# Kernel tuning notes

Measured on AMD Instinct MI355X. Metric: run time of the kernel, lower is better.

The kernel has to match this reference:

```python
import jax, jax.numpy as jnp
import numpy as np

D = 128  # node_dim (hardcoded in the torch module)


def _bn(x, g, b, eps=1e-5):
    # BatchNorm1d in training mode: per-batch mean / biased variance
    m = x.mean(0)
    v = x.var(0)
    return (x - m) * jax.lax.rsqrt(v + eps) * g + b


def setup_inputs() -> dict:
    key = jax.random.key(0)
    ks = jax.random.split(key, 16)
    N, E, ED = 4096, 16384, 16
    node = jax.random.normal(ks[0], (N, D), jnp.float32)
    edge = jax.random.normal(ks[1], (E, ED), jnp.float32)
    hidden = jax.random.normal(ks[2], (1, N, D), jnp.float32)
    edge_index = jax.random.randint(ks[3], (E, 2), 0, N)

    def lin(k, o, i):
        return jax.random.normal(k, (o, i), jnp.float32) / np.sqrt(i).astype(np.float32)

    W1 = lin(ks[4], 256, ED)
    W2 = lin(ks[5], 256, 256)
    W3 = lin(ks[6], 128, 256)
    W4 = lin(ks[7], D * D, 128)
    g1, b1 = jnp.ones(256), jnp.zeros(256)
    g2, b2 = jnp.ones(256), jnp.zeros(256)
    g3, b3 = jnp.ones(128), jnp.zeros(128)
    g4, b4 = jnp.ones(D * D), jnp.zeros(D * D)
    lim = 1.0 / np.sqrt(D).astype(np.float32)
    bias = jax.random.uniform(ks[8], (D,), jnp.float32, -lim, lim)
    W_ih = lin(ks[9], 3 * D, D)
    W_hh = lin(ks[10], 3 * D, D)
    b_ih = jnp.zeros(3 * D)
    b_hh = jnp.zeros(3 * D)
    return dict(node=node, edge_index=edge_index, edge=edge, hidden=hidden,
                W1=W1, g1=g1, b1=b1, W2=W2, g2=g2, b2=b2, W3=W3, g3=g3, b3=b3,
                W4=W4, g4=g4, b4=b4, bias=bias, W_ih=W_ih, W_hh=W_hh,
                b_ih=b_ih, b_hh=b_hh)


def reference(node, edge_index, edge, hidden, W1, g1, b1, W2, g2, b2,
              W3, g3, b3, W4, g4, b4, bias, W_ih, W_hh, b_ih, b_hh):
    N = node.shape[0]
    E = edge.shape[0]
    h0 = hidden[0]  # [N, D]
    src, dst = edge_index[:, 0], edge_index[:, 1]

    # edge encoder -> per-edge [D, D] weight matrix
    x = jax.nn.relu(_bn(edge @ W1.T, g1, b1))
    x = jax.nn.relu(_bn(x @ W2.T, g2, b2))
    x = jax.nn.relu(_bn(x @ W3.T, g3, b3))
    w = _bn(x @ W4.T, g4, b4).reshape(E, D, D)

    # gather source nodes, per-edge vector-matrix product
    x_i = node[src]                               # [E, D]
    msg = jnp.einsum('ed,edk->ek', x_i, w)        # [E, D]

    # scatter-mean over destination nodes
    sums = jax.ops.segment_sum(msg, dst, num_segments=N)
    cnt = jax.ops.segment_sum(jnp.ones((E, 1), msg.dtype), dst, num_segments=N)
    message = sums / jnp.maximum(cnt, 1.0)
    m = jax.nn.relu(message + bias)               # [N, D]

    # single-step GRU (PyTorch gate order r, z, n)
    gi = m @ W_ih.T + b_ih
    gh = h0 @ W_hh.T + b_hh
    r = jax.nn.sigmoid(gi[:, :D] + gh[:, :D])
    z = jax.nn.sigmoid(gi[:, D:2 * D] + gh[:, D:2 * D])
    n = jnp.tanh(gi[:, 2 * D:] + r * gh[:, 2 * D:])
    hn = (1.0 - z) * n + z * h0                   # [N, D]
    return hn, hn[None]
```

## Files before the change

kernel.cpp:

```cpp
#include <hip/hip_runtime.h>

#define EPS 1e-5f

typedef _Float16 half8 __attribute__((ext_vector_type(8)));
typedef float f32x16 __attribute__((ext_vector_type(16)));

__global__ __launch_bounds__(256) void gemm_abt(const float* __restrict__ A,
                                                const float* __restrict__ B,
                                                float* __restrict__ C,
                                                int M, int N, int K,
                                                float* __restrict__ osum,
                                                float* __restrict__ osq) {
  __shared__ float As[16][68];
  __shared__ float Bs[16][68];
  const int t = threadIdx.x;
  const int tx = t & 15, ty = t >> 4;
  const int m0 = blockIdx.y * 64, n0 = blockIdx.x * 64;
  float acc[4][4] = {};
  for (int k0 = 0; k0 < K; k0 += 16) {
    __syncthreads();
    {
      const int r = t >> 2;
      const int kk = (t & 3) << 2;
      float4 av = *(const float4*)&A[(size_t)(m0 + r) * K + k0 + kk];
      As[kk + 0][r] = av.x; As[kk + 1][r] = av.y;
      As[kk + 2][r] = av.z; As[kk + 3][r] = av.w;
      float4 bv = *(const float4*)&B[(size_t)(n0 + r) * K + k0 + kk];
      Bs[kk + 0][r] = bv.x; Bs[kk + 1][r] = bv.y;
      Bs[kk + 2][r] = bv.z; Bs[kk + 3][r] = bv.w;
    }
    __syncthreads();
#pragma unroll
    for (int kk = 0; kk < 16; ++kk) {
      float4 a = *(const float4*)&As[kk][ty << 2];
      float4 b = *(const float4*)&Bs[kk][tx << 2];
      float av[4] = {a.x, a.y, a.z, a.w};
      float bv[4] = {b.x, b.y, b.z, b.w};
#pragma unroll
      for (int i = 0; i < 4; ++i)
#pragma unroll
        for (int j = 0; j < 4; ++j) acc[i][j] += av[i] * bv[j];
    }
  }
#pragma unroll
  for (int i = 0; i < 4; ++i) {
    float4 o = make_float4(acc[i][0], acc[i][1], acc[i][2], acc[i][3]);
    *(float4*)&C[(size_t)(m0 + (ty << 2) + i) * N + n0 + (tx << 2)] = o;
  }
  __syncthreads();
  float* sred = (float*)As;
  if (t < 128) sred[t] = 0.f;
  __syncthreads();
#pragma unroll
  for (int j = 0; j < 4; ++j) {
    float s = 0.f, sq = 0.f;
#pragma unroll
    for (int i = 0; i < 4; ++i) {
      float v = acc[i][j];
      s += v; sq += v * v;
    }
    atomicAdd(&sred[((tx << 2) + j) * 2 + 0], s);
    atomicAdd(&sred[((tx << 2) + j) * 2 + 1], sq);
  }
  __syncthreads();
  if (t < 64) {
    atomicAdd(&osum[n0 + t], sred[t * 2]);
    atomicAdd(&osq[n0 + t], sred[t * 2 + 1]);
  }
}

template <int TRANS, bool STATS>
__global__ __launch_bounds__(256) void gemm16(const float* __restrict__ A,
                                              const float* __restrict__ B,
                                              float* __restrict__ C,
                                              int lda, int ldb, int ldc, int K,
                                              const float* __restrict__ s1,
                                              const float* __restrict__ s2,
                                              const float* __restrict__ g,
                                              const float* __restrict__ b,
                                              float invM,
                                              float* __restrict__ osum,
                                              float* __restrict__ osq) {
  __shared__ _Float16 As[128 * 64];
  __shared__ _Float16 Bs[128 * 64];
  __shared__ float scL[256], shL[256];
  const int t = threadIdx.x;
  const int m0 = blockIdx.y * 128, n0 = blockIdx.x * 128;
  const int w = t >> 6, l = t & 63;
  const int wm = w >> 1, wn = w & 1;
  const int lr = l & 31, lg = l >> 5;
  if (TRANS == 1) {
    if (t < K) {
      float mean = s1[t] * invM;
      float var = s2[t] * invM - mean * mean;
      float sc = g[t] * rsqrtf(var + EPS);
      scL[t] = sc;
      shL[t] = b[t] - mean * sc;
    }
  }
  f32x16 acc[2][2];
#pragma unroll
  for (int i = 0; i < 2; ++i)
#pragma unroll
    for (int j = 0; j < 2; ++j) acc[i][j] = (f32x16){0.f};
  for (int k0 = 0; k0 < K; k0 += 64) {
    __syncthreads();
#pragma unroll
    for (int i = 0; i < 4; ++i) {
      const int gq = i * 256 + t;
      const int f = gq >> 6, lp = gq & 63;
      const int row = (f >> 2) * 32 + (lp & 31);
      const int c = (f & 3) * 16 + (lp >> 5) * 8;
      const float* ap = A + (size_t)(m0 + row) * lda + k0 + c;
      float4 a4 = *(const float4*)ap, b4 = *(const float4*)(ap + 4);
      float va[8] = {a4.x, a4.y, a4.z, a4.w, b4.x, b4.y, b4.z, b4.w};
      if (TRANS == 1) {
#pragma unroll
        for (int j = 0; j < 8; ++j)
          va[j] = fmaxf(va[j] * scL[k0 + c + j] + shL[k0 + c + j], 0.f);
      }
      half8 h;
#pragma unroll
      for (int j = 0; j < 8; ++j) h[j] = (_Float16)va[j];
      *(half8*)(As + (size_t)gq * 8) = h;
      const float* bp = B + (size_t)(n0 + row) * ldb + k0 + c;
      float4 e4 = *(const float4*)bp, f4 = *(const float4*)(bp + 4);
      half8 hb;
      hb[0] = (_Float16)e4.x; hb[1] = (_Float16)e4.y; hb[2] = (_Float16)e4.z; hb[3] = (_Float16)e4.w;
      hb[4] = (_Float16)f4.x; hb[5] = (_Float16)f4.y; hb[6] = (_Float16)f4.z; hb[7] = (_Float16)f4.w;
      *(half8*)(Bs + (size_t)gq * 8) = hb;
    }
    __syncthreads();
#pragma unroll
    for (int ks = 0; ks < 4; ++ks) {
      half8 af[2], bf[2];
#pragma unroll
      for (int mb = 0; mb < 2; ++mb) {
        af[mb] = *(const half8*)(As + (size_t)(((wm * 2 + mb) * 4 + ks) * 64 + l) * 8);
        bf[mb] = *(const half8*)(Bs + (size_t)(((wn * 2 + mb) * 4 + ks) * 64 + l) * 8);
      }
#pragma unroll
      for (int mb = 0; mb < 2; ++mb)
#pragma unroll
        for (int nb = 0; nb < 2; ++nb)
          acc[mb][nb] = __builtin_amdgcn_mfma_f32_32x32x16_f16(af[mb], bf[nb], acc[mb][nb], 0, 0, 0);
    }
  }
#pragma unroll
  for (int mb = 0; mb < 2; ++mb)
#pragma unroll
    for (int nb = 0; nb < 2; ++nb)
#pragma unroll
      for (int r = 0; r < 16; ++r) {
        const int row = m0 + wm * 64 + mb * 32 + (r & 3) + 8 * (r >> 2) + 4 * lg;
        const int col = n0 + wn * 64 + nb * 32 + lr;
        C[(size_t)row * ldc + col] = acc[mb][nb][r];
      }
  if (STATS) {
    __syncthreads();
    float* sred = (float*)As;
    if (t < 256) sred[t] = 0.f;
    __syncthreads();
#pragma unroll
    for (int nb = 0; nb < 2; ++nb) {
      float s = 0.f, sq = 0.f;
#pragma unroll
      for (int mb = 0; mb < 2; ++mb)
#pragma unroll
        for (int r = 0; r < 16; ++r) {
          float v = acc[mb][nb][r];
          s += v; sq += v * v;
        }
      const int cl = wn * 64 + nb * 32 + lr;
      atomicAdd(&sred[cl * 2 + 0], s);
      atomicAdd(&sred[cl * 2 + 1], sq);
    }
    __syncthreads();
    if (t < 128) {
      atomicAdd(&osum[n0 + t], sred[t * 2]);
      atomicAdd(&osq[n0 + t], sred[t * 2 + 1]);
    }
  }
}

__global__ __launch_bounds__(256) void gram_kernel(const float* __restrict__ y3,
                                                   float* __restrict__ part,
                                                   const float* __restrict__ s3sum,
                                                   const float* __restrict__ s3sq,
                                                   const float* __restrict__ g3,
                                                   const float* __restrict__ b3,
                                                   float invE,
                                                   float* __restrict__ colsum) {
  __shared__ float xL[128 * 132];
  __shared__ float scL[128], shL[128];
  const int t = threadIdx.x, tx = t & 15, ty = t >> 4;
  if (t < 128) {
    float mean = s3sum[t] * invE;
    float var = s3sq[t] * invE - mean * mean;
    float sc = g3[t] * rsqrtf(var + EPS);
    scL[t] = sc;
    shL[t] = b3[t] - mean * sc;
  }
  __syncthreads();
  const int r0 = blockIdx.x * 128;
#pragma unroll
  for (int i = 0; i < 16; ++i) {
    int f4 = t + i * 256;
    int r = f4 >> 5;
    int c4 = (f4 & 31) << 2;
    float4 v = *(const float4*)&y3[(size_t)(r0 + r) * 128 + c4];
    v.x = fmaxf(v.x * scL[c4 + 0] + shL[c4 + 0], 0.f);
    v.y = fmaxf(v.y * scL[c4 + 1] + shL[c4 + 1], 0.f);
    v.z = fmaxf(v.z * scL[c4 + 2] + shL[c4 + 2], 0.f);
    v.w = fmaxf(v.w * scL[c4 + 3] + shL[c4 + 3], 0.f);
    *(float4*)&xL[r * 132 + c4] = v;
  }
  __syncthreads();
  float acc[8][8] = {};
  float csum[8] = {};
  for (int r = 0; r < 128; ++r) {
    float4 a0 = *(const float4*)&xL[r * 132 + ty * 8];
    float4 a1 = *(const float4*)&xL[r * 132 + ty * 8 + 4];
    float4 b0 = *(const float4*)&xL[r * 132 + tx * 8];
    float4 b1 = *(const float4*)&xL[r * 132 + tx * 8 + 4];
    float a[8] = {a0.x, a0.y, a0.z, a0.w, a1.x, a1.y, a1.z, a1.w};
    float b[8] = {b0.x, b0.y, b0.z, b0.w, b1.x, b1.y, b1.z, b1.w};
#pragma unroll
    for (int i = 0; i < 8; ++i)
#pragma unroll
      for (int j = 0; j < 8; ++j) acc[i][j] += a[i] * b[j];
    if (tx == ty) {
#pragma unroll
      for (int i = 0; i < 8; ++i) csum[i] += a[i];
    }
  }
  float* base = part + (size_t)blockIdx.x * 16384;
#pragma unroll
  for (int i = 0; i < 8; ++i)
#pragma unroll
    for (int j = 0; j < 8; ++j)
      base[(ty * 8 + i) * 128 + tx * 8 + j] = acc[i][j];
  if (tx == ty) {
#pragma unroll
    for (int i = 0; i < 8; ++i) atomicAdd(&colsum[ty * 8 + i], csum[i]);
  }
}

__global__ __launch_bounds__(256) void gram_reduce(const float* __restrict__ part,
                                                   float* __restrict__ out) {
  int idx = blockIdx.x * 256 + threadIdx.x;
  float s = 0.f;
  for (int b = 0; b < 128; ++b) s += part[(size_t)b * 16384 + idx];
  out[idx] = s;
}

__global__ __launch_bounds__(256) void w4_finalize(const float* __restrict__ W4,
                                                   const float* __restrict__ U,
                                                   const float* __restrict__ colsum3,
                                                   const float* __restrict__ g4,
                                                   const float* __restrict__ b4,
                                                   _Float16* __restrict__ BTf,
                                                   float* __restrict__ t4,
                                                   float invM) {
  const int r = (blockIdx.x * 256 + threadIdx.x) >> 6;
  const int lane = threadIdx.x & 63;
  const float* wp = W4 + (size_t)r * 128;
  const float* up = U + (size_t)r * 128;
  float p1 = 0.f, p2 = 0.f;
#pragma unroll
  for (int c0 = 0; c0 < 128; c0 += 64) {
    float wv = wp[c0 + lane];
    p1 += up[c0 + lane] * wv;
    p2 += colsum3[c0 + lane] * wv;
  }
#pragma unroll
  for (int off = 32; off > 0; off >>= 1) {
    p1 += __shfl_down(p1, off);
    p2 += __shfl_down(p2, off);
  }
  p1 = __shfl(p1, 0);
  p2 = __shfl(p2, 0);
  float m4 = p2 * invM;
  float q = p1 * invM;
  float s = g4[r] * rsqrtf(q - m4 * m4 + EPS);
  if (lane == 0) t4[r] = b4[r] - m4 * s;
  const int kout = r & 127, d = r >> 7;
  if (lane < 16) {
    const int ks = lane >> 1, lg = lane & 1;
    const float* cp = wp + lane * 8;
    float4 va = *(const float4*)cp, vb = *(const float4*)(cp + 4);
    half8 h;
    h[0] = (_Float16)(s * va.x); h[1] = (_Float16)(s * va.y);
    h[2] = (_Float16)(s * va.z); h[3] = (_Float16)(s * va.w);
    h[4] = (_Float16)(s * vb.x); h[5] = (_Float16)(s * vb.y);
    h[6] = (_Float16)(s * vb.z); h[7] = (_Float16)(s * vb.w);
    size_t off16 = (size_t)d * 16384 +
                   (size_t)((((kout >> 5) * 8 + ks) * 64) + (kout & 31) + lg * 32) * 8;
    *(half8*)(BTf + off16) = h;
  }
}

__global__ __launch_bounds__(256, 2) void zgemm(const float* __restrict__ y3,
                                                const float* __restrict__ node,
                                                const int* __restrict__ eidx,
                                                const _Float16* __restrict__ BTf,
                                                const float* __restrict__ Tn,
                                                const float* __restrict__ s3sum,
                                                const float* __restrict__ s3sq,
                                                const float* __restrict__ g3,
                                                const float* __restrict__ b3,
                                                float invE,
                                                float* __restrict__ sums) {
  __shared__ __align__(16) _Float16 Bs[2][16384];
  __shared__ _Float16 xiL[32 * 128];
  __shared__ float scL[128], shL[128];
  const int t = threadIdx.x;
  const int e0 = blockIdx.y * 128;
  const int d0 = blockIdx.x * 32;
  const int w = t >> 6, l = t & 63;
  const int wm = w >> 1, wn = w & 1;
  const int lr = l & 31, lg = l >> 5;
  if (t < 128) {
    float mean = s3sum[t] * invE;
    float var = s3sq[t] * invE - mean * mean;
    float sc = g3[t] * rsqrtf(var + EPS);
    scL[t] = sc;
    shL[t] = b3[t] - mean * sc;
  }
  {
    const int e = t >> 1, db = (t & 1) * 16;
    const int src = eidx[(e0 + e) * 2];
    const float* np = node + (size_t)src * 128 + d0 + db;
#pragma unroll
    for (int j = 0; j < 16; j += 4) {
      float4 v = *(const float4*)(np + j);
      xiL[(db + j + 0) * 128 + e] = (_Float16)v.x;
      xiL[(db + j + 1) * 128 + e] = (_Float16)v.y;
      xiL[(db + j + 2) * 128 + e] = (_Float16)v.z;
      xiL[(db + j + 3) * 128 + e] = (_Float16)v.w;
    }
  }
  half8 st[8];
  {
    const _Float16* p = BTf + (size_t)d0 * 16384 + (size_t)t * 8;
#pragma unroll
    for (int j = 0; j < 8; ++j) st[j] = *(const half8*)(p + j * 2048);
  }
  __syncthreads();
  half8 xf[2][8];
#pragma unroll
  for (int mb = 0; mb < 2; ++mb) {
    const float* xp = y3 + (size_t)(e0 + wm * 64 + mb * 32 + lr) * 128 + lg * 8;
#pragma unroll
    for (int ks = 0; ks < 8; ++ks) {
      const int c = ks * 16 + lg * 8;
      float4 a = *(const float4*)(xp + ks * 16);
      float4 b = *(const float4*)(xp + ks * 16 + 4);
      float va[8] = {a.x, a.y, a.z, a.w, b.x, b.y, b.z, b.w};
      half8 h;
#pragma unroll
      for (int j = 0; j < 8; ++j)
        h[j] = (_Float16)fmaxf(va[j] * scL[c + j] + shL[c + j], 0.f);
      xf[mb][ks] = h;
    }
  }
  f32x16 acc00 = (f32x16){0.f}, acc01 = (f32x16){0.f};
  f32x16 acc10 = (f32x16){0.f}, acc11 = (f32x16){0.f};

  for (int dt = 0; dt < 32; ++dt) {
    _Float16* bs = &Bs[dt & 1][0];
#pragma unroll
    for (int j = 0; j < 8; ++j) *(half8*)(bs + t * 8 + j * 2048) = st[j];
    if (dt < 31) {
      const _Float16* p = BTf + (size_t)(d0 + dt + 1) * 16384 + (size_t)t * 8;
#pragma unroll
      for (int j = 0; j < 8; ++j) st[j] = *(const half8*)(p + j * 2048);
    }
    asm volatile("s_waitcnt lgkmcnt(0)" ::: "memory");
    __builtin_amdgcn_s_barrier();
    const _Float16 xv0 = xiL[dt * 128 + wm * 64 + lr];
    const _Float16 xv1 = xiL[dt * 128 + wm * 64 + 32 + lr];
    const half8 xb0 = {xv0, xv0, xv0, xv0, xv0, xv0, xv0, xv0};
    const half8 xb1 = {xv1, xv1, xv1, xv1, xv1, xv1, xv1, xv1};
    __builtin_amdgcn_s_setprio(1);
#pragma unroll
    for (int ks = 0; ks < 8; ++ks) {
      half8 b0 = *(const half8*)(bs + (size_t)(((wn * 2 + 0) * 8 + ks) * 64 + l) * 8);
      half8 b1 = *(const half8*)(bs + (size_t)(((wn * 2 + 1) * 8 + ks) * 64 + l) * 8);
      half8 a0 = xf[0][ks] * xb0;
      half8 a1 = xf[1][ks] * xb1;
      acc00 = __builtin_amdgcn_mfma_f32_32x32x16_f16(a0, b0, acc00, 0, 0, 0);
      acc01 = __builtin_amdgcn_mfma_f32_32x32x16_f16(a0, b1, acc01, 0, 0, 0);
      acc10 = __builtin_amdgcn_mfma_f32_32x32x16_f16(a1, b0, acc10, 0, 0, 0);
      acc11 = __builtin_amdgcn_mfma_f32_32x32x16_f16(a1, b1, acc11, 0, 0, 0);
    }
    __builtin_amdgcn_s_setprio(0);
  }
  const bool add_t = (blockIdx.x == 0);
#pragma unroll
  for (int r = 0; r < 16; ++r) {
    const int rl = (r & 3) + 8 * (r >> 2) + 4 * lg;
    const int eA = e0 + wm * 64 + rl;
    const int eB = eA + 32;
    const int dA = eidx[eA * 2 + 1], sA = eidx[eA * 2];
    const int dB = eidx[eB * 2 + 1], sB = eidx[eB * 2];
    const int c0 = wn * 64 + lr;
    float v00 = acc00[r], v01 = acc01[r], v10 = acc10[r], v11 = acc11[r];
    if (add_t) {
      v00 += Tn[(size_t)sA * 128 + c0];
      v01 += Tn[(size_t)sA * 128 + c0 + 32];
      v10 += Tn[(size_t)sB * 128 + c0];
      v11 += Tn[(size_t)sB * 128 + c0 + 32];
    }
    atomicAdd(&sums[(size_t)dA * 128 + c0], v00);
    atomicAdd(&sums[(size_t)dA * 128 + c0 + 32], v01);
    atomicAdd(&sums[(size_t)dB * 128 + c0], v10);
    atomicAdd(&sums[(size_t)dB * 128 + c0 + 32], v11);
  }
}

__global__ __launch_bounds__(128) void t4n_kernel(const float* __restrict__ node,
                                                  const float* __restrict__ t4,
                                                  float* __restrict__ Tn,
                                                  const int* __restrict__ eidx,
                                                  float* __restrict__ cnt, int E) {
  __shared__ float nodeL[8][128];
  const int k = threadIdx.x;
  const int n0 = blockIdx.x * 8;
  {
    int e = blockIdx.x * 32 + k;
    if (k < 32 && e < E) atomicAdd(&cnt[eidx[e * 2 + 1]], 1.0f);
  }
#pragma unroll
  for (int j = 0; j < 8; ++j) nodeL[j][k] = node[(size_t)(n0 + j) * 128 + k];
  __syncthreads();
  float acc[8] = {};
  for (int d = 0; d < 128; ++d) {
    float wv = t4[d * 128 + k];
#pragma unroll
    for (int j = 0; j < 8; ++j) acc[j] += nodeL[j][d] * wv;
  }
#pragma unroll
  for (int j = 0; j < 8; ++j) Tn[(size_t)(n0 + j) * 128 + k] = acc[j];
}

__global__ __launch_bounds__(256) void gru_gates(const float* __restrict__ sums,
                                                 const float* __restrict__ cnt,
                                                 const float* __restrict__ bias,
                                                 const float* __restrict__ h0,
                                                 const float* __restrict__ Wih,
                                                 const float* __restrict__ Whh,
                                                 float* __restrict__ gi,
                                                 float* __restrict__ gh) {
  __shared__ _Float16 As[128 * 64];
  __shared__ _Float16 Bs[128 * 64];
  const bool isgh = blockIdx.x >= 3;
  const float* A = isgh ? h0 : sums;
  const float* B = isgh ? Whh : Wih;
  float* C = isgh ? gh : gi;
  const int n0 = (isgh ? blockIdx.x - 3 : blockIdx.x) * 128;
  const int m0 = blockIdx.y * 128;
  const int t = threadIdx.x;
  const int w = t >> 6, l = t & 63;
  const int wm = w >> 1, wn = w & 1;
  const int lr = l & 31, lg = l >> 5;
  f32x16 acc[2][2];
#pragma unroll
  for (int i = 0; i < 2; ++i)
#pragma unroll
    for (int j = 0; j < 2; ++j) acc[i][j] = (f32x16){0.f};
  for (int k0 = 0; k0 < 128; k0 += 64) {
    __syncthreads();
#pragma unroll
    for (int i = 0; i < 4; ++i) {
      const int gq = i * 256 + t;
      const int f = gq >> 6, lp = gq & 63;
      const int row = (f >> 2) * 32 + (lp & 31);
      const int c = (f & 3) * 16 + (lp >> 5) * 8;
      const float* ap = A + (size_t)(m0 + row) * 128 + k0 + c;
      float4 a4 = *(const float4*)ap, b4 = *(const float4*)(ap + 4);
      float va[8] = {a4.x, a4.y, a4.z, a4.w, b4.x, b4.y, b4.z, b4.w};
      if (!isgh) {
        float rc = 1.f / fmaxf(cnt[m0 + row], 1.f);
#pragma unroll
        for (int j = 0; j < 8; ++j) va[j] = fmaxf(va[j] * rc + bias[k0 + c + j], 0.f);
      }
      half8 h;
#pragma unroll
      for (int j = 0; j < 8; ++j) h[j] = (_Float16)va[j];
      *(half8*)(As + (size_t)gq * 8) = h;
      const float* bp = B + (size_t)(n0 + row) * 128 + k0 + c;
      float4 e4 = *(const float4*)bp, f4 = *(const float4*)(bp + 4);
      half8 hb;
      hb[0] = (_Float16)e4.x; hb[1] = (_Float16)e4.y; hb[2] = (_Float16)e4.z; hb[3] = (_Float16)e4.w;
      hb[4] = (_Float16)f4.x; hb[5] = (_Float16)f4.y; hb[6] = (_Float16)f4.z; hb[7] = (_Float16)f4.w;
      *(half8*)(Bs + (size_t)gq * 8) = hb;
    }
    __syncthreads();
#pragma unroll
    for (int ks = 0; ks < 4; ++ks) {
      half8 af[2], bf[2];
#pragma unroll
      for (int mb = 0; mb < 2; ++mb) {
        af[mb] = *(const half8*)(As + (size_t)(((wm * 2 + mb) * 4 + ks) * 64 + l) * 8);
        bf[mb] = *(const half8*)(Bs + (size_t)(((wn * 2 + mb) * 4 + ks) * 64 + l) * 8);
      }
#pragma unroll
      for (int mb = 0; mb < 2; ++mb)
#pragma unroll
        for (int nb = 0; nb < 2; ++nb)
          acc[mb][nb] = __builtin_amdgcn_mfma_f32_32x32x16_f16(af[mb], bf[nb], acc[mb][nb], 0, 0, 0);
    }
  }
#pragma unroll
  for (int mb = 0; mb < 2; ++mb)
#pragma unroll
    for (int nb = 0; nb < 2; ++nb)
#pragma unroll
      for (int r = 0; r < 16; ++r) {
        const int row = m0 + wm * 64 + mb * 32 + (r & 3) + 8 * (r >> 2) + 4 * lg;
        const int col = n0 + wn * 64 + nb * 32 + lr;
        C[(size_t)row * 384 + col] = acc[mb][nb][r];
      }
}

__global__ __launch_bounds__(256) void gru_finalize(const float* __restrict__ gi,
                                                    const float* __restrict__ gh,
                                                    const float* __restrict__ h0,
                                                    const float* __restrict__ bih,
                                                    const float* __restrict__ bhh,
                                                    float* __restrict__ out, int Nn) {
  int idx = blockIdx.x * 256 + threadIdx.x;
  int n = idx >> 7, k = idx & 127;
  const float* gin = gi + (size_t)n * 384;
  const float* ghn = gh + (size_t)n * 384;
  float r = 1.f / (1.f + expf(-(gin[k] + bih[k] + ghn[k] + bhh[k])));
  float z = 1.f / (1.f + expf(-(gin[128 + k] + bih[128 + k] + ghn[128 + k] + bhh[128 + k])));
  float nn = tanhf(gin[256 + k] + bih[256 + k] + r * (ghn[256 + k] + bhh[256 + k]));
  float h = h0[idx];
  float hn = (1.f - z) * nn + z * h;
  out[idx] = hn;
  out[idx + (size_t)Nn * 128] = hn;
}

extern "C" void kernel_launch(void* const* d_in, const int* in_sizes, int n_in,
                              void* d_out, int out_size, void* d_ws, size_t ws_size,
                              hipStream_t stream) {
  const float* node = (const float*)d_in[0];
  const int* eidx = (const int*)d_in[1];
  const float* edge = (const float*)d_in[2];
  const float* hidden = (const float*)d_in[3];
  const float* W1 = (const float*)d_in[4];
  const float* g1 = (const float*)d_in[5];
  const float* b1 = (const float*)d_in[6];
  const float* W2 = (const float*)d_in[7];
  const float* g2 = (const float*)d_in[8];
  const float* b2 = (const float*)d_in[9];
  const float* W3 = (const float*)d_in[10];
  const float* g3 = (const float*)d_in[11];
  const float* b3 = (const float*)d_in[12];
  const float* W4 = (const float*)d_in[13];
  const float* g4 = (const float*)d_in[14];
  const float* b4 = (const float*)d_in[15];
  const float* bias = (const float*)d_in[16];
  const float* Wih = (const float*)d_in[17];
  const float* Whh = (const float*)d_in[18];
  const float* bih = (const float*)d_in[19];
  const float* bhh = (const float*)d_in[20];
  float* out = (float*)d_out;

  const int Nn = in_sizes[0] / 128;
  const int E = in_sizes[2] / 16;
  const float invE = 1.0f / (float)E;

  float* ws = (float*)d_ws;
  float* ybuf1 = ws + 0;
  float* ybuf2 = ws + 4194304;
  float* y3buf = ws + 8388608;
  _Float16* BTf = (_Float16*)(ws + 10485760);
  float* t4 = ws + 11534336;
  float* stats = ws + 11550720;
  float* G3 = ws + 11552512;
  float* sums = ws + 11568896;
  float* cnt = ws + 12093184;
  float* Tn = ws + 12097280;
  float* stat1 = stats, *stat2 = stats + 512, *stat3 = stats + 1024;
  float* colsum3 = stats + 1536;
  float* gpart = ybuf1;
  float* U = ybuf2;
  float* gi = ybuf2;
  float* gh = ybuf2 + 1572864;

  hipMemsetAsync(stats, 0, 1664 * sizeof(float), stream);
  hipMemsetAsync(sums, 0, ((size_t)Nn * 128 + Nn) * sizeof(float), stream);

  gemm_abt<<<dim3(4, E / 64), 256, 0, stream>>>(edge, W1, ybuf1, E, 256, 16, stat1, stat1 + 256);
  gemm16<1, true><<<dim3(2, E / 128), 256, 0, stream>>>(ybuf1, W2, ybuf2, 256, 256, 256, 256,
                                                        stat1, stat1 + 256, g1, b1, invE,
                                                        stat2, stat2 + 256);
  gemm16<1, true><<<dim3(1, E / 128), 256, 0, stream>>>(ybuf2, W3, y3buf, 256, 256, 128, 256,
                                                        stat2, stat2 + 256, g2, b2, invE,
                                                        stat3, stat3 + 256);

  gram_kernel<<<E / 128, 256, 0, stream>>>(y3buf, gpart, stat3, stat3 + 256, g3, b3, invE,
                                           colsum3);
  gram_reduce<<<64, 256, 0, stream>>>(gpart, G3);

  gemm16<0, false><<<dim3(1, 16384 / 128), 256, 0, stream>>>(W4, G3, U, 128, 128, 128, 128,
                                                             nullptr, nullptr, nullptr, nullptr,
                                                             0.f, nullptr, nullptr);
  w4_finalize<<<16384 / 4, 256, 0, stream>>>(W4, U, colsum3, g4, b4, BTf, t4, invE);
  t4n_kernel<<<Nn / 8, 128, 0, stream>>>(node, t4, Tn, eidx, cnt, E);

  zgemm<<<dim3(4, E / 128), 256, 0, stream>>>(y3buf, node, eidx, BTf, Tn,
                                              stat3, stat3 + 256, g3, b3, invE, sums);

  gru_gates<<<dim3(6, Nn / 128), 256, 0, stream>>>(sums, cnt, bias, hidden, Wih, Whh, gi, gh);
  gru_finalize<<<Nn * 128 / 256, 256, 0, stream>>>(gi, gh, hidden, bih, bhh, out, Nn);
}
```

Before: 254.9 us.

## Store edge-encoder intermediates in fp16 and restructure zgemm B-tile prefetch

The edge-encoder activations y1, y2 and y3 are now written as fp16 instead of fp32, and the downstream GEMM, gram and zgemm kernels read them as fp16. This halves the global traffic for these intermediates. Separately, zgemm now prefetches B tiles two steps ahead and interleaves the LDS stores for the next tile with the MFMA loop, leaving a single barrier per iteration. The trade-offs are rounding error in the pre-BatchNorm activations (pre-activations are cast to fp16 before normalization) and extra register pressure.

New measurement: 239.9 us. 5.9% less time.

```diff
diff --git a/kernel.cpp b/kernel.cpp
--- a/kernel.cpp
+++ b/kernel.cpp
@@ -3,11 +3,12 @@
 #define EPS 1e-5f
 
 typedef _Float16 half8 __attribute__((ext_vector_type(8)));
+typedef _Float16 half4 __attribute__((ext_vector_type(4)));
 typedef float f32x16 __attribute__((ext_vector_type(16)));
 
 __global__ __launch_bounds__(256) void gemm_abt(const float* __restrict__ A,
                                                 const float* __restrict__ B,
-                                                float* __restrict__ C,
+                                                _Float16* __restrict__ C,
                                                 int M, int N, int K,
                                                 float* __restrict__ osum,
                                                 float* __restrict__ osq) {
@@ -44,8 +45,10 @@
   }
 #pragma unroll
   for (int i = 0; i < 4; ++i) {
-    float4 o = make_float4(acc[i][0], acc[i][1], acc[i][2], acc[i][3]);
-    *(float4*)&C[(size_t)(m0 + (ty << 2) + i) * N + n0 + (tx << 2)] = o;
+    half4 o;
+    o[0] = (_Float16)acc[i][0]; o[1] = (_Float16)acc[i][1];
+    o[2] = (_Float16)acc[i][2]; o[3] = (_Float16)acc[i][3];
+    *(half4*)&C[(size_t)(m0 + (ty << 2) + i) * N + n0 + (tx << 2)] = o;
   }
   __syncthreads();
   float* sred = (float*)As;
@@ -69,10 +72,10 @@
   }
 }
 
-template <int TRANS, bool STATS>
-__global__ __launch_bounds__(256) void gemm16(const float* __restrict__ A,
+template <int TRANS, bool STATS, bool AH, bool CH>
+__global__ __launch_bounds__(256) void gemm16(const void* __restrict__ Ap,
                                               const float* __restrict__ B,
-                                              float* __restrict__ C,
+                                              void* __restrict__ Cp,
                                               int lda, int ldb, int ldc, int K,
                                               const float* __restrict__ s1,
                                               const float* __restrict__ s2,
@@ -111,9 +114,18 @@
       const int f = gq >> 6, lp = gq & 63;
       const int row = (f >> 2) * 32 + (lp & 31);
       const int c = (f & 3) * 16 + (lp >> 5) * 8;
-      const float* ap = A + (size_t)(m0 + row) * lda + k0 + c;
-      float4 a4 = *(const float4*)ap, b4 = *(const float4*)(ap + 4);
-      float va[8] = {a4.x, a4.y, a4.z, a4.w, b4.x, b4.y, b4.z, b4.w};
+      float va[8];
+      if (AH) {
+        const _Float16* ap = (const _Float16*)Ap + (size_t)(m0 + row) * lda + k0 + c;
+        half8 av = *(const half8*)ap;
+#pragma unroll
+        for (int j = 0; j < 8; ++j) va[j] = (float)av[j];
+      } else {
+        const float* ap = (const float*)Ap + (size_t)(m0 + row) * lda + k0 + c;
+        float4 a4 = *(const float4*)ap, b4 = *(const float4*)(ap + 4);
+        va[0] = a4.x; va[1] = a4.y; va[2] = a4.z; va[3] = a4.w;
+        va[4] = b4.x; va[5] = b4.y; va[6] = b4.z; va[7] = b4.w;
+      }
       if (TRANS == 1) {
 #pragma unroll
         for (int j = 0; j < 8; ++j)
@@ -154,7 +166,8 @@
       for (int r = 0; r < 16; ++r) {
         const int row = m0 + wm * 64 + mb * 32 + (r & 3) + 8 * (r >> 2) + 4 * lg;
         const int col = n0 + wn * 64 + nb * 32 + lr;
-        C[(size_t)row * ldc + col] = acc[mb][nb][r];
+        if (CH) ((_Float16*)Cp)[(size_t)row * ldc + col] = (_Float16)acc[mb][nb][r];
+        else ((float*)Cp)[(size_t)row * ldc + col] = acc[mb][nb][r];
       }
   if (STATS) {
     __syncthreads();
@@ -183,7 +196,7 @@
   }
 }
 
-__global__ __launch_bounds__(256) void gram_kernel(const float* __restrict__ y3,
+__global__ __launch_bounds__(256) void gram_kernel(const _Float16* __restrict__ y3,
                                                    float* __restrict__ part,
                                                    const float* __restrict__ s3sum,
                                                    const float* __restrict__ s3sq,
@@ -208,11 +221,12 @@
     int f4 = t + i * 256;
     int r = f4 >> 5;
     int c4 = (f4 & 31) << 2;
-    float4 v = *(const float4*)&y3[(size_t)(r0 + r) * 128 + c4];
-    v.x = fmaxf(v.x * scL[c4 + 0] + shL[c4 + 0], 0.f);
-    v.y = fmaxf(v.y * scL[c4 + 1] + shL[c4 + 1], 0.f);
-    v.z = fmaxf(v.z * scL[c4 + 2] + shL[c4 + 2], 0.f);
-    v.w = fmaxf(v.w * scL[c4 + 3] + shL[c4 + 3], 0.f);
+    half4 hv = *(const half4*)&y3[(size_t)(r0 + r) * 128 + c4];
+    float4 v;
+    v.x = fmaxf((float)hv[0] * scL[c4 + 0] + shL[c4 + 0], 0.f);
+    v.y = fmaxf((float)hv[1] * scL[c4 + 1] + shL[c4 + 1], 0.f);
+    v.z = fmaxf((float)hv[2] * scL[c4 + 2] + shL[c4 + 2], 0.f);
+    v.w = fmaxf((float)hv[3] * scL[c4 + 3] + shL[c4 + 3], 0.f);
     *(float4*)&xL[r * 132 + c4] = v;
   }
   __syncthreads();
@@ -300,7 +314,7 @@
   }
 }
 
-__global__ __launch_bounds__(256, 2) void zgemm(const float* __restrict__ y3,
+__global__ __launch_bounds__(256, 2) void zgemm(const _Float16* __restrict__ y3,
                                                 const float* __restrict__ node,
                                                 const int* __restrict__ eidx,
                                                 const _Float16* __restrict__ BTf,
@@ -346,21 +360,26 @@
 #pragma unroll
     for (int j = 0; j < 8; ++j) st[j] = *(const half8*)(p + j * 2048);
   }
+#pragma unroll
+  for (int j = 0; j < 8; ++j) *(half8*)(&Bs[0][0] + t * 8 + j * 2048) = st[j];
+  {
+    const _Float16* p = BTf + (size_t)(d0 + 1) * 16384 + (size_t)t * 8;
+#pragma unroll
+    for (int j = 0; j < 8; ++j) st[j] = *(const half8*)(p + j * 2048);
+  }
   __syncthreads();
   half8 xf[2][8];
 #pragma unroll
   for (int mb = 0; mb < 2; ++mb) {
-    const float* xp = y3 + (size_t)(e0 + wm * 64 + mb * 32 + lr) * 128 + lg * 8;
+    const _Float16* xp = y3 + (size_t)(e0 + wm * 64 + mb * 32 + lr) * 128 + lg * 8;
 #pragma unroll
     for (int ks = 0; ks < 8; ++ks) {
       const int c = ks * 16 + lg * 8;
-      float4 a = *(const float4*)(xp + ks * 16);
-      float4 b = *(const float4*)(xp + ks * 16 + 4);
-      float va[8] = {a.x, a.y, a.z, a.w, b.x, b.y, b.z, b.w};
+      half8 hv = *(const half8*)(xp + ks * 16);
       half8 h;
 #pragma unroll
       for (int j = 0; j < 8; ++j)
-        h[j] = (_Float16)fmaxf(va[j] * scL[c + j] + shL[c + j], 0.f);
+        h[j] = (_Float16)fmaxf((float)hv[j] * scL[c + j] + shL[c + j], 0.f);
       xf[mb][ks] = h;
     }
   }
@@ -368,16 +387,8 @@
   f32x16 acc10 = (f32x16){0.f}, acc11 = (f32x16){0.f};
 
   for (int dt = 0; dt < 32; ++dt) {
-    _Float16* bs = &Bs[dt & 1][0];
-#pragma unroll
-    for (int j = 0; j < 8; ++j) *(half8*)(bs + t * 8 + j * 2048) = st[j];
-    if (dt < 31) {
-      const _Float16* p = BTf + (size_t)(d0 + dt + 1) * 16384 + (size_t)t * 8;
-#pragma unroll
-      for (int j = 0; j < 8; ++j) st[j] = *(const half8*)(p + j * 2048);
-    }
-    asm volatile("s_waitcnt lgkmcnt(0)" ::: "memory");
-    __builtin_amdgcn_s_barrier();
+    const _Float16* bs = &Bs[dt & 1][0];
+    _Float16* bsn = &Bs[(dt + 1) & 1][0];
     const _Float16 xv0 = xiL[dt * 128 + wm * 64 + lr];
     const _Float16 xv1 = xiL[dt * 128 + wm * 64 + 32 + lr];
     const half8 xb0 = {xv0, xv0, xv0, xv0, xv0, xv0, xv0, xv0};
@@ -387,6 +398,7 @@
     for (int ks = 0; ks < 8; ++ks) {
       half8 b0 = *(const half8*)(bs + (size_t)(((wn * 2 + 0) * 8 + ks) * 64 + l) * 8);
       half8 b1 = *(const half8*)(bs + (size_t)(((wn * 2 + 1) * 8 + ks) * 64 + l) * 8);
+      if (dt < 31) *(half8*)(bsn + t * 8 + ks * 2048) = st[ks];
       half8 a0 = xf[0][ks] * xb0;
       half8 a1 = xf[1][ks] * xb1;
       acc00 = __builtin_amdgcn_mfma_f32_32x32x16_f16(a0, b0, acc00, 0, 0, 0);
@@ -395,6 +407,13 @@
       acc11 = __builtin_amdgcn_mfma_f32_32x32x16_f16(a1, b1, acc11, 0, 0, 0);
     }
     __builtin_amdgcn_s_setprio(0);
+    if (dt < 30) {
+      const _Float16* p = BTf + (size_t)(d0 + dt + 2) * 16384 + (size_t)t * 8;
+#pragma unroll
+      for (int j = 0; j < 8; ++j) st[j] = *(const half8*)(p + j * 2048);
+    }
+    asm volatile("s_waitcnt lgkmcnt(0)" ::: "memory");
+    __builtin_amdgcn_s_barrier();
   }
   const bool add_t = (blockIdx.x == 0);
 #pragma unroll
@@ -574,9 +593,11 @@
   const float invE = 1.0f / (float)E;
 
   float* ws = (float*)d_ws;
-  float* ybuf1 = ws + 0;
+  _Float16* y1h = (_Float16*)(ws + 0);
+  float* gpart = ws + 0;
   float* ybuf2 = ws + 4194304;
-  float* y3buf = ws + 8388608;
+  _Float16* y2h = (_Float16*)ybuf2;
+  _Float16* y3h = (_Float16*)(ws + 8388608);
   _Float16* BTf = (_Float16*)(ws + 10485760);
   float* t4 = ws + 11534336;
   float* stats = ws + 11550720;
@@ -586,7 +607,6 @@
   float* Tn = ws + 12097280;
   float* stat1 = stats, *stat2 = stats + 512, *stat3 = stats + 1024;
   float* colsum3 = stats + 1536;
-  float* gpart = ybuf1;
   float* U = ybuf2;
   float* gi = ybuf2;
   float* gh = ybuf2 + 1572864;
@@ -594,25 +614,22 @@
   hipMemsetAsync(stats, 0, 1664 * sizeof(float), stream);
   hipMemsetAsync(sums, 0, ((size_t)Nn * 128 + Nn) * sizeof(float), stream);
 
-  gemm_abt<<<dim3(4, E / 64), 256, 0, stream>>>(edge, W1, ybuf1, E, 256, 16, stat1, stat1 + 256);
-  gemm16<1, true><<<dim3(2, E / 128), 256, 0, stream>>>(ybuf1, W2, ybuf2, 256, 256, 256, 256,
-                                                        stat1, stat1 + 256, g1, b1, invE,
-                                                        stat2, stat2 + 256);
-  gemm16<1, true><<<dim3(1, E / 128), 256, 0, stream>>>(ybuf2, W3, y3buf, 256, 256, 128, 256,
-                                                        stat2, stat2 + 256, g2, b2, invE,
-                                                        stat3, stat3 + 256);
-
-  gram_kernel<<<E / 128, 256, 0, stream>>>(y3buf, gpart, stat3, stat3 + 256, g3, b3, invE,
+  gemm_abt<<<dim3(4, E / 64), 256, 0, stream>>>(edge, W1, y1h, E, 256, 16, stat1, stat1 + 256);
+  gemm16<1, true, true, true><<<dim3(2, E / 128), 256, 0, stream>>>(
+      y1h, W2, y2h, 256, 256, 256, 256, stat1, stat1 + 256, g1, b1, invE, stat2, stat2 + 256);
+  gemm16<1, true, true, true><<<dim3(1, E / 128), 256, 0, stream>>>(
+      y2h, W3, y3h, 256, 256, 128, 256, stat2, stat2 + 256, g2, b2, invE, stat3, stat3 + 256);
+
+  gram_kernel<<<E / 128, 256, 0, stream>>>(y3h, gpart, stat3, stat3 + 256, g3, b3, invE,
                                            colsum3);
   gram_reduce<<<64, 256, 0, stream>>>(gpart, G3);
 
-  gemm16<0, false><<<dim3(1, 16384 / 128), 256, 0, stream>>>(W4, G3, U, 128, 128, 128, 128,
-                                                             nullptr, nullptr, nullptr, nullptr,
-                                                             0.f, nullptr, nullptr);
+  gemm16<0, false, false, false><<<dim3(1, 16384 / 128), 256, 0, stream>>>(
+      W4, G3, U, 128, 128, 128, 128, nullptr, nullptr, nullptr, nullptr, 0.f, nullptr, nullptr);
   w4_finalize<<<16384 / 4, 256, 0, stream>>>(W4, U, colsum3, g4, b4, BTf, t4, invE);
   t4n_kernel<<<Nn / 8, 128, 0, stream>>>(node, t4, Tn, eidx, cnt, E);
 
-  zgemm<<<dim3(4, E / 128), 256, 0, stream>>>(y3buf, node, eidx, BTf, Tn,
+  zgemm<<<dim3(4, E / 128), 256, 0, stream>>>(y3h, node, eidx, BTf, Tn,
                                               stat3, stat3 + 256, g3, b3, invE, sums);
 
   gru_gates<<<dim3(6, Nn / 128), 256, 0, stream>>>(sums, cnt, bias, hidden, Wih, Whh, gi, gh);
```
